# Kernel optimization log

Hardware: AMD Instinct MI355X
Metric: run time of the kernel (lower is better)

The kernel has to match this reference:

```python
import jax, jax.numpy as jnp
import numpy as np

B, T, C = 2, 2048, 2048
H, KVH, HD = 16, 4, 128  # heads, kv heads, head_dim
G = H // KVH             # GQA group size
THETA = 10000.0


def _rope_cos_sin(t, hd, dtype):
    inv_freq = 1.0 / (THETA ** (jnp.arange(0, hd, 2, dtype=jnp.float32) / hd))
    pos = jnp.arange(t, dtype=jnp.float32)
    freqs = pos[:, None] * inv_freq[None, :]          # [T, hd/2]
    emb = jnp.concatenate([freqs, freqs], axis=-1)    # [T, hd]
    return jnp.cos(emb).astype(dtype), jnp.sin(emb).astype(dtype)


def _rotate_half(x):
    x1, x2 = jnp.split(x, 2, axis=-1)
    return jnp.concatenate([-x2, x1], axis=-1)


def setup_inputs() -> dict:
    key = jax.random.key(0)
    ks = jax.random.split(key, 5)
    s_in = 1.0 / np.sqrt(C)
    return {
        "x": jax.random.normal(ks[0], (B, T, C), jnp.float32),
        "wq": jax.random.normal(ks[1], (C, H * HD), jnp.float32) * s_in,
        "bq": jnp.zeros((H * HD,), jnp.float32),
        "wk": jax.random.normal(ks[2], (C, KVH * HD), jnp.float32) * s_in,
        "bk": jnp.zeros((KVH * HD,), jnp.float32),
        "wv": jax.random.normal(ks[3], (C, KVH * HD), jnp.float32) * s_in,
        "bv": jnp.zeros((KVH * HD,), jnp.float32),
        "wo": jax.random.normal(ks[4], (H * HD, C), jnp.float32) * (1.0 / np.sqrt(H * HD)),
    }


def reference(x, wq, bq, wk, bk, wv, bv, wo):
    b, t, c = x.shape
    q = (x @ wq + bq).reshape(b, t, H, HD).transpose(0, 2, 1, 3)    # [B,H,T,hd]
    k = (x @ wk + bk).reshape(b, t, KVH, HD).transpose(0, 2, 1, 3)  # [B,KVH,T,hd]
    v = (x @ wv + bv).reshape(b, t, KVH, HD).transpose(0, 2, 1, 3)

    cos, sin = _rope_cos_sin(t, HD, x.dtype)  # [T,hd]
    q = q * cos + _rotate_half(q) * sin
    k = k * cos + _rotate_half(k) * sin

    # GQA: group query heads over kv heads
    qg = q.reshape(b, KVH, G, t, HD)
    scale = 1.0 / np.sqrt(HD)
    scores = jnp.einsum('bkgtd,bksd->bkgts', qg, k) * scale  # [B,KVH,G,T,T]
    causal = jnp.tril(jnp.ones((t, t), bool))
    scores = jnp.where(causal, scores, jnp.finfo(scores.dtype).min)
    attn = jax.nn.softmax(scores, axis=-1)
    out = jnp.einsum('bkgts,bksd->bkgtd', attn, v)            # [B,KVH,G,T,hd]
    out = out.reshape(b, H, t, HD).transpose(0, 2, 1, 3).reshape(b, t, H * HD)
    return out @ wo
```

## Files before the change

### kernel.cpp

```cpp
#include <hip/hip_runtime.h>
#include <hip/hip_bf16.h>
#include <math.h>

#define B_ 2
#define T_ 2048
#define C_ 2048
#define H_ 16
#define KVH_ 4
#define HD_ 128
#define G_ (H_ / KVH_)
#define MROWS (B_ * T_)
#define NQKV (H_ * HD_ + 2 * KVH_ * HD_)
#define KOFF (H_ * HD_)
#define VOFF (H_ * HD_ + KVH_ * HD_)

typedef __hip_bfloat16 bf16;
typedef short bf16x8 __attribute__((ext_vector_type(8)));
typedef short bf16x4 __attribute__((ext_vector_type(4)));
typedef float f32x4 __attribute__((ext_vector_type(4)));

__device__ __forceinline__ void gload_lds16(const void* g, void* l) {
  __builtin_amdgcn_global_load_lds(
      (const __attribute__((address_space(1))) unsigned int*)g,
      (__attribute__((address_space(3))) unsigned int*)l, 16, 0, 0);
}

static __device__ __forceinline__ f32x4 mfma16(bf16x4 a, bf16x4 b, f32x4 c) {
#if __has_builtin(__builtin_amdgcn_mfma_f32_16x16x16_bf16)
  return __builtin_amdgcn_mfma_f32_16x16x16_bf16(a, b, c, 0, 0, 0);
#else
  return __builtin_amdgcn_mfma_f32_16x16x16bf16_1k(a, b, c, 0, 0, 0);
#endif
}

static __device__ __forceinline__ short f2bf(float x) {
  unsigned u = __builtin_bit_cast(unsigned, x);
  u += 0x7FFFu + ((u >> 16) & 1u);
  return (short)(u >> 16);
}

static __device__ __forceinline__ float fexp2(float x) {
#if __has_builtin(__builtin_amdgcn_exp2f)
  return __builtin_amdgcn_exp2f(x);
#else
  return exp2f(x);
#endif
}

__global__ void cast_bf16_kernel(const float* __restrict__ in, bf16* __restrict__ out, int n) {
  int i = (blockIdx.x * 256 + threadIdx.x) * 4;
  if (i >= n) return;
  float4 v = *(const float4*)(in + i);
  out[i + 0] = __float2bfloat16(v.x);
  out[i + 1] = __float2bfloat16(v.y);
  out[i + 2] = __float2bfloat16(v.z);
  out[i + 3] = __float2bfloat16(v.w);
}

__global__ __launch_bounds__(256) void transpose_cast(const float* __restrict__ in,
                                                      bf16* __restrict__ out,
                                                      int R, int Ccols) {
  __shared__ float t[32][33];
  const int tx = threadIdx.x & 31, ty = threadIdx.x >> 5;
  const int r0 = blockIdx.y * 32, c0 = blockIdx.x * 32;
#pragma unroll
  for (int it = 0; it < 4; ++it)
    t[ty + 8 * it][tx] = in[(size_t)(r0 + ty + 8 * it) * Ccols + c0 + tx];
  __syncthreads();
#pragma unroll
  for (int it = 0; it < 4; ++it)
    out[(size_t)(c0 + ty + 8 * it) * R + r0 + tx] = __float2bfloat16(t[tx][ty + 8 * it]);
}

__global__ __launch_bounds__(256) void transpose_cast_qkvw(
    const float* __restrict__ wq, const float* __restrict__ wk,
    const float* __restrict__ wv, bf16* __restrict__ outT) {
  __shared__ float t[32][33];
  const int tx = threadIdx.x & 31, ty = threadIdx.x >> 5;
  const int r0 = blockIdx.y * 32;
  const int c0 = blockIdx.x * 32;
  const float* src;
  int nn, ld;
  if (c0 < KOFF)      { src = wq; nn = c0;        ld = 2048; }
  else if (c0 < VOFF) { src = wk; nn = c0 - KOFF; ld = 512; }
  else                { src = wv; nn = c0 - VOFF; ld = 512; }
#pragma unroll
  for (int it = 0; it < 4; ++it)
    t[ty + 8 * it][tx] = src[(size_t)(r0 + ty + 8 * it) * ld + nn + tx];
  __syncthreads();
#pragma unroll
  for (int it = 0; it < 4; ++it)
    outT[(size_t)(c0 + ty + 8 * it) * 2048 + r0 + tx] = __float2bfloat16(t[tx][ty + 8 * it]);
}

__global__ __launch_bounds__(256) void transpose_v(const bf16* __restrict__ qkv,
                                                   bf16* __restrict__ vt) {
  __shared__ bf16 t[32][33];
  const int tx = threadIdx.x & 31, ty = threadIdx.x >> 5;
  const int b = blockIdx.z >> 2, kvh = blockIdx.z & 3;
  const int t0 = blockIdx.x * 32, d0 = blockIdx.y * 32;
#pragma unroll
  for (int it = 0; it < 4; ++it)
    t[ty + 8 * it][tx] =
        qkv[(size_t)(b * T_ + t0 + ty + 8 * it) * NQKV + VOFF + kvh * HD_ + d0 + tx];
  __syncthreads();
#pragma unroll
  for (int it = 0; it < 4; ++it)
    vt[((size_t)((b * KVH_ + kvh) * HD_) + d0 + ty + 8 * it) * T_ + t0 + tx] =
        t[tx][ty + 8 * it];
}

__global__ void rope_bf16(bf16* __restrict__ buf, int ld, int col0, int nheads) {
  const int row = blockIdx.x / nheads;
  const int h = blockIdx.x % nheads;
  const int t = row % T_;
  const int d = threadIdx.x;
  bf16* rp = buf + (size_t)row * ld + col0 + h * HD_;
  float vd = __bfloat162float(rp[d]);
  float vp = __bfloat162float(rp[d ^ 64]);
  __syncthreads();
  const int i = d & 63;
  float invf = fexp2(-(float)i * (13.287712379549449f / 64.0f));
  float ang = (float)t * invf;
  float s, c;
  __sincosf(ang, &s, &c);
  rp[d] = __float2bfloat16((d < 64) ? (vd * c - vp * s) : (vd * c + vp * s));
}

template <bool BF16OUT>
__global__ __launch_bounds__(256, 2) void gemm_mfma(
    const bf16* __restrict__ A, const bf16* __restrict__ Bt, void* __restrict__ Cout,
    const float* __restrict__ bq, const float* __restrict__ bk2,
    const float* __restrict__ bv2, int M, int N, int K) {
  __shared__ __align__(16) bf16 As[128 * 32];
  __shared__ __align__(16) bf16 Bs[128 * 32];
  const int tid = threadIdx.x;
  const int w = tid >> 6, lane = tid & 63;
  const int colL = lane & 15, quad = lane >> 4;
  const int wm = w & 1, wn = w >> 1;
  const int r0 = blockIdx.y * 128, c0 = blockIdx.x * 128;

  f32x4 acc[4][4];
  const f32x4 zero = {0.f, 0.f, 0.f, 0.f};
#pragma unroll
  for (int mt = 0; mt < 4; ++mt)
#pragma unroll
    for (int nt = 0; nt < 4; ++nt) acc[mt][nt] = zero;

  for (int k0 = 0; k0 < K; k0 += 32) {
    __syncthreads();
#pragma unroll
    for (int it = 0; it < 2; ++it) {
      const int seg = it * 4 + w;
      const int idx = seg * 64 + lane;
      const int row = idx >> 2, off = idx & 3;
      gload_lds16(A + (size_t)(r0 + row) * K + k0 + off * 8, &As[seg * 512]);
      gload_lds16(Bt + (size_t)(c0 + row) * K + k0 + off * 8, &Bs[seg * 512]);
    }
    __syncthreads();
    bf16x8 af[4], bfv[4];
#pragma unroll
    for (int mt = 0; mt < 4; ++mt)
      af[mt] = *(const bf16x8*)&As[(wm * 64 + mt * 16 + colL) * 32 + quad * 8];
#pragma unroll
    for (int nt = 0; nt < 4; ++nt)
      bfv[nt] = *(const bf16x8*)&Bs[(wn * 64 + nt * 16 + colL) * 32 + quad * 8];
#pragma unroll
    for (int mt = 0; mt < 4; ++mt)
#pragma unroll
      for (int nt = 0; nt < 4; ++nt)
        acc[mt][nt] =
            __builtin_amdgcn_mfma_f32_16x16x32_bf16(af[mt], bfv[nt], acc[mt][nt], 0, 0, 0);
  }

#pragma unroll
  for (int nt = 0; nt < 4; ++nt) {
    const int c = c0 + wn * 64 + nt * 16 + colL;
    float bias = 0.f;
    if (bq) bias = (c < KOFF) ? bq[c] : (c < VOFF ? bk2[c - KOFF] : bv2[c - VOFF]);
#pragma unroll
    for (int mt = 0; mt < 4; ++mt) {
#pragma unroll
      for (int i = 0; i < 4; ++i) {
        const int r = r0 + wm * 64 + mt * 16 + quad * 4 + i;
        const float v = acc[mt][nt][i] + bias;
        if (BF16OUT)
          ((bf16*)Cout)[(size_t)r * N + c] = __float2bfloat16(v);
        else
          ((float*)Cout)[(size_t)r * N + c] = v;
      }
    }
  }
}

#define FA_SCL2 (0.08838834764831845f * 1.4426950408889634f)
#define FA_M2 16.0f

__global__ __launch_bounds__(128, 2) void flash_mfma5(
    const bf16* __restrict__ qkv, const bf16* __restrict__ vt, bf16* __restrict__ ao) {
  __shared__ __align__(16) char smem[32768];
  bf16* Kb0 = (bf16*)smem;
  bf16* Kb1 = (bf16*)(smem + 8192);
  bf16* Vb0 = (bf16*)(smem + 16384);
  bf16* Vb1 = (bf16*)(smem + 24576);

  const int id = blockIdx.x;
  const int hb = id >> 5;
  const int qq = id & 31;
  const int qt = (qq & 1) ? (qq >> 1) : (31 - (qq >> 1));
  const int h = hb & 15, b = hb >> 4;
  const int kvh = h >> 2;

  const int tid = threadIdx.x;
  const int w = tid >> 6, lane = tid & 63;
  const int colL = lane & 15, quad = lane >> 4;
  const int myq0 = qt * 64 + 32 * w;

  const bf16* kg = qkv + (size_t)(b * T_) * NQKV + KOFF + kvh * HD_;
  const bf16* vg = vt + (size_t)((b * KVH_ + kvh) * HD_) * T_;

  auto stageKV = [&](int tile, bf16* kl, bf16* vl) {
    const int s0k = tile * 32;
#pragma unroll
    for (int j = 0; j < 4; ++j) {
      const int s = 4 * w + j;
      const int row = s * 4 + quad;
      const int g = colL ^ (row & 7);
      gload_lds16(kg + (size_t)(s0k + row) * NQKV + g * 8, kl + s * 512);
    }
#pragma unroll
    for (int j = 0; j < 4; ++j) {
      const int s = 4 * w + j;
      const int row = s * 16 + (lane >> 2);
      const int g = (lane & 3) ^ ((row >> 1) & 3);
      gload_lds16(vg + (size_t)row * T_ + s0k + g * 8, vl + s * 512);
    }
  };

  bf16x8 qf[2][4];
  {
    const bf16* qgw = qkv + (size_t)(b * T_ + myq0) * NQKV + h * HD_;
#pragma unroll
    for (int mq = 0; mq < 2; ++mq)
#pragma unroll
      for (int c = 0; c < 4; ++c)
        qf[mq][c] = *(const bf16x8*)(qgw + (size_t)(mq * 16 + colL) * NQKV + c * 32 + quad * 8);
  }

  f32x4 o[2][8];
  const f32x4 zero = {0.f, 0.f, 0.f, 0.f};
#pragma unroll
  for (int mq = 0; mq < 2; ++mq)
#pragma unroll
    for (int ht = 0; ht < 8; ++ht) o[mq][ht] = zero;
  float l_[2] = {0.f, 0.f};

  const int nkv = 2 * qt + 2;
  stageKV(0, Kb0, Vb0);
  asm volatile("s_waitcnt vmcnt(0)\n\ts_barrier" ::: "memory");

  for (int tt = 0; tt < nkv; ++tt) {
    const bf16* Ks = (tt & 1) ? Kb1 : Kb0;
    const bf16* Vs = (tt & 1) ? Vb1 : Vb0;
    if (tt + 1 < nkv) stageKV(tt + 1, (tt & 1) ? Kb0 : Kb1, (tt & 1) ? Vb0 : Vb1);

    const int s0 = tt * 32;
    if (s0 < myq0 + 32) {
      f32x4 s_[2][2];
      s_[0][0] = zero; s_[0][1] = zero; s_[1][0] = zero; s_[1][1] = zero;
#pragma unroll
      for (int c = 0; c < 4; ++c) {
        const int ch = ((c * 4 + quad) ^ (colL & 7)) * 8;
        bf16x8 kf0 = *(const bf16x8*)(Ks + (size_t)colL * 128 + ch);
        bf16x8 kf1 = *(const bf16x8*)(Ks + (size_t)(16 + colL) * 128 + ch);
#pragma unroll
        for (int mq = 0; mq < 2; ++mq) {
          s_[0][mq] = __builtin_amdgcn_mfma_f32_16x16x32_bf16(kf0, qf[mq][c], s_[0][mq], 0, 0, 0);
          s_[1][mq] = __builtin_amdgcn_mfma_f32_16x16x32_bf16(kf1, qf[mq][c], s_[1][mq], 0, 0, 0);
        }
      }

      bf16x4 pf[2][2];
      if (s0 >= myq0) {
#pragma unroll
        for (int kt = 0; kt < 2; ++kt)
#pragma unroll
          for (int mq = 0; mq < 2; ++mq) {
            const int qcol = myq0 + mq * 16 + colL;
            const int kb = s0 + kt * 16 + quad * 4;
            float pv[4];
#pragma unroll
            for (int i = 0; i < 4; ++i) {
              float e = fexp2(fmaf(s_[kt][mq][i], FA_SCL2, -FA_M2));
              pv[i] = (kb + i <= qcol) ? e : 0.f;
            }
            l_[mq] += (pv[0] + pv[1]) + (pv[2] + pv[3]);
            pf[kt][mq] = (bf16x4){f2bf(pv[0]), f2bf(pv[1]), f2bf(pv[2]), f2bf(pv[3])};
          }
      } else {
#pragma unroll
        for (int kt = 0; kt < 2; ++kt)
#pragma unroll
          for (int mq = 0; mq < 2; ++mq) {
            float pv[4];
#pragma unroll
            for (int i = 0; i < 4; ++i)
              pv[i] = fexp2(fmaf(s_[kt][mq][i], FA_SCL2, -FA_M2));
            l_[mq] += (pv[0] + pv[1]) + (pv[2] + pv[3]);
            pf[kt][mq] = (bf16x4){f2bf(pv[0]), f2bf(pv[1]), f2bf(pv[2]), f2bf(pv[3])};
          }
      }

#pragma unroll
      for (int ht = 0; ht < 8; ++ht) {
        const int row = ht * 16 + colL;
#pragma unroll
        for (int kt = 0; kt < 2; ++kt) {
          bf16x4 vf = *(const bf16x4*)(Vs + (size_t)row * 32 +
                                       (((kt * 2 + (quad >> 1)) ^ ((row >> 1) & 3)) * 8) +
                                       (quad & 1) * 4);
#pragma unroll
          for (int mq = 0; mq < 2; ++mq) o[mq][ht] = mfma16(vf, pf[kt][mq], o[mq][ht]);
        }
      }
    }
    asm volatile("s_waitcnt vmcnt(0)\n\ts_barrier" ::: "memory");
  }

#pragma unroll
  for (int mq = 0; mq < 2; ++mq) {
    l_[mq] += __shfl_xor(l_[mq], 16);
    l_[mq] += __shfl_xor(l_[mq], 32);
    const float rl = 1.f / l_[mq];
    const size_t rbase = (size_t)(b * T_ + myq0 + mq * 16 + colL) * (H_ * HD_) + h * HD_;
#pragma unroll
    for (int ht = 0; ht < 8; ++ht) {
      bf16x4 ov;
#pragma unroll
      for (int i = 0; i < 4; ++i) ov[i] = f2bf(o[mq][ht][i] * rl);
      *(bf16x4*)(ao + rbase + ht * 16 + quad * 4) = ov;
    }
  }
}

extern "C" void kernel_launch(void* const* d_in, const int* in_sizes, int n_in,
                              void* d_out, int out_size, void* d_ws, size_t ws_size,
                              hipStream_t stream) {
  (void)in_sizes; (void)n_in; (void)out_size; (void)ws_size;
  const float* x  = (const float*)d_in[0];
  const float* wq = (const float*)d_in[1];
  const float* bq = (const float*)d_in[2];
  const float* wk = (const float*)d_in[3];
  const float* bk = (const float*)d_in[4];
  const float* wv = (const float*)d_in[5];
  const float* bv = (const float*)d_in[6];
  const float* wo = (const float*)d_in[7];
  float* out = (float*)d_out;

  char* ws = (char*)d_ws;
  bf16* xb    = (bf16*)ws;
  bf16* wqkvT = (bf16*)(ws + (16u << 20));
  bf16* woT   = (bf16*)(ws + (28u << 20));
  bf16* qkv   = (bf16*)(ws + (36u << 20));
  bf16* vt    = (bf16*)(ws + (60u << 20));

  cast_bf16_kernel<<<dim3(MROWS * C_ / 1024), dim3(256), 0, stream>>>(x, xb, MROWS * C_);

  transpose_cast_qkvw<<<dim3(96, 64), dim3(256), 0, stream>>>(wq, wk, wv, wqkvT);
  transpose_cast<<<dim3(64, 64), dim3(256), 0, stream>>>(wo, woT, 2048, 2048);

  gemm_mfma<true><<<dim3(NQKV / 128, MROWS / 128), dim3(256), 0, stream>>>(
      xb, wqkvT, qkv, bq, bk, bv, MROWS, NQKV, C_);

  rope_bf16<<<dim3(MROWS * H_), dim3(128), 0, stream>>>(qkv, NQKV, 0, H_);
  rope_bf16<<<dim3(MROWS * KVH_), dim3(128), 0, stream>>>(qkv, NQKV, KOFF, KVH_);

  transpose_v<<<dim3(T_ / 32, HD_ / 32, B_ * KVH_), dim3(256), 0, stream>>>(qkv, vt);

  bf16* ao = xb;
  flash_mfma5<<<dim3(1024), dim3(128), 0, stream>>>(qkv, vt, ao);

  gemm_mfma<false><<<dim3(C_ / 128, MROWS / 128), dim3(256), 0, stream>>>(
      ao, woT, out, nullptr, nullptr, nullptr, MROWS, C_, KOFF);
}
```

Baseline: 354.1 us.

## Pair causal query tiles per block, triple-buffer KV loads, merge RoPE launches

The flash-attention kernel now has each block handle two query tiles, qq and 31-qq, in sequence. This balances causal work per block and halves the grid to 512 blocks. KV staging moves from double to triple buffering with a partial vmcnt wait, so two tiles are in flight, and occupancy hints rise to 4 blocks/CU with 48KB LDS. The Q and K RoPE launches are merged into one launch covering 20 heads per row. The trade-offs are more LDS per block and fewer blocks, which could cut parallelism on a device with many CUs.

New measurement: 355.2 us. Within noise of the previous version (+0.3%).

```diff
diff --git a/kernel.cpp b/kernel.cpp
--- a/kernel.cpp
+++ b/kernel.cpp
@@ -110,12 +110,12 @@
         t[tx][ty + 8 * it];
 }
 
-__global__ void rope_bf16(bf16* __restrict__ buf, int ld, int col0, int nheads) {
-  const int row = blockIdx.x / nheads;
-  const int h = blockIdx.x % nheads;
+__global__ void rope_bf16(bf16* __restrict__ buf) {
+  const int row = blockIdx.x / 20;
+  const int hh = blockIdx.x % 20;
   const int t = row % T_;
   const int d = threadIdx.x;
-  bf16* rp = buf + (size_t)row * ld + col0 + h * HD_;
+  bf16* rp = buf + (size_t)row * NQKV + hh * HD_;
   float vd = __bfloat162float(rp[d]);
   float vp = __bfloat162float(rp[d ^ 64]);
   __syncthreads();
@@ -196,30 +196,26 @@
 #define FA_SCL2 (0.08838834764831845f * 1.4426950408889634f)
 #define FA_M2 16.0f
 
-__global__ __launch_bounds__(128, 2) void flash_mfma5(
+__global__ __launch_bounds__(128, 4) void flash_mfma6(
     const bf16* __restrict__ qkv, const bf16* __restrict__ vt, bf16* __restrict__ ao) {
-  __shared__ __align__(16) char smem[32768];
-  bf16* Kb0 = (bf16*)smem;
-  bf16* Kb1 = (bf16*)(smem + 8192);
-  bf16* Vb0 = (bf16*)(smem + 16384);
-  bf16* Vb1 = (bf16*)(smem + 24576);
+  __shared__ __align__(16) char smem[49152];
 
   const int id = blockIdx.x;
-  const int hb = id >> 5;
-  const int qq = id & 31;
-  const int qt = (qq & 1) ? (qq >> 1) : (31 - (qq >> 1));
+  const int hb = id >> 4;
+  const int qq = id & 15;
   const int h = hb & 15, b = hb >> 4;
   const int kvh = h >> 2;
 
   const int tid = threadIdx.x;
   const int w = tid >> 6, lane = tid & 63;
   const int colL = lane & 15, quad = lane >> 4;
-  const int myq0 = qt * 64 + 32 * w;
 
   const bf16* kg = qkv + (size_t)(b * T_) * NQKV + KOFF + kvh * HD_;
   const bf16* vg = vt + (size_t)((b * KVH_ + kvh) * HD_) * T_;
 
-  auto stageKV = [&](int tile, bf16* kl, bf16* vl) {
+  auto stageKV = [&](int tile, char* base) {
+    bf16* kl = (bf16*)base;
+    bf16* vl = (bf16*)(base + 8192);
     const int s0k = tile * 32;
 #pragma unroll
     for (int j = 0; j < 4; ++j) {
@@ -237,108 +233,125 @@
     }
   };
 
-  bf16x8 qf[2][4];
-  {
-    const bf16* qgw = qkv + (size_t)(b * T_ + myq0) * NQKV + h * HD_;
+#pragma unroll 1
+  for (int pass = 0; pass < 2; ++pass) {
+    const int qt = pass ? (31 - qq) : qq;
+    const int myq0 = qt * 64 + 32 * w;
+    const int nkv = 2 * qt + 2;
+
+    bf16x8 qf[2][4];
+    {
+      const bf16* qgw = qkv + (size_t)(b * T_ + myq0) * NQKV + h * HD_;
+#pragma unroll
+      for (int mq = 0; mq < 2; ++mq)
+#pragma unroll
+        for (int c = 0; c < 4; ++c)
+          qf[mq][c] = *(const bf16x8*)(qgw + (size_t)(mq * 16 + colL) * NQKV + c * 32 + quad * 8);
+    }
+
+    f32x4 o[2][8];
+    const f32x4 zero = {0.f, 0.f, 0.f, 0.f};
 #pragma unroll
     for (int mq = 0; mq < 2; ++mq)
 #pragma unroll
-      for (int c = 0; c < 4; ++c)
-        qf[mq][c] = *(const bf16x8*)(qgw + (size_t)(mq * 16 + colL) * NQKV + c * 32 + quad * 8);
-  }
-
-  f32x4 o[2][8];
-  const f32x4 zero = {0.f, 0.f, 0.f, 0.f};
-#pragma unroll
-  for (int mq = 0; mq < 2; ++mq)
-#pragma unroll
-    for (int ht = 0; ht < 8; ++ht) o[mq][ht] = zero;
-  float l_[2] = {0.f, 0.f};
-
-  const int nkv = 2 * qt + 2;
-  stageKV(0, Kb0, Vb0);
-  asm volatile("s_waitcnt vmcnt(0)\n\ts_barrier" ::: "memory");
-
-  for (int tt = 0; tt < nkv; ++tt) {
-    const bf16* Ks = (tt & 1) ? Kb1 : Kb0;
-    const bf16* Vs = (tt & 1) ? Vb1 : Vb0;
-    if (tt + 1 < nkv) stageKV(tt + 1, (tt & 1) ? Kb0 : Kb1, (tt & 1) ? Vb0 : Vb1);
-
-    const int s0 = tt * 32;
-    if (s0 < myq0 + 32) {
-      f32x4 s_[2][2];
-      s_[0][0] = zero; s_[0][1] = zero; s_[1][0] = zero; s_[1][1] = zero;
-#pragma unroll
-      for (int c = 0; c < 4; ++c) {
-        const int ch = ((c * 4 + quad) ^ (colL & 7)) * 8;
-        bf16x8 kf0 = *(const bf16x8*)(Ks + (size_t)colL * 128 + ch);
-        bf16x8 kf1 = *(const bf16x8*)(Ks + (size_t)(16 + colL) * 128 + ch);
-#pragma unroll
-        for (int mq = 0; mq < 2; ++mq) {
-          s_[0][mq] = __builtin_amdgcn_mfma_f32_16x16x32_bf16(kf0, qf[mq][c], s_[0][mq], 0, 0, 0);
-          s_[1][mq] = __builtin_amdgcn_mfma_f32_16x16x32_bf16(kf1, qf[mq][c], s_[1][mq], 0, 0, 0);
+      for (int ht = 0; ht < 8; ++ht) o[mq][ht] = zero;
+    float l_[2] = {0.f, 0.f};
+
+    stageKV(0, smem);
+    stageKV(1, smem + 16384);
+    asm volatile("s_waitcnt vmcnt(8)\n\ts_barrier" ::: "memory");
+
+    int rb = 0, sb = 2;
+#pragma unroll 1
+    for (int tt = 0; tt < nkv; ++tt) {
+      const bool pre = (tt + 2 < nkv);
+      if (pre) stageKV(tt + 2, smem + sb * 16384);
+      const bf16* Ks = (const bf16*)(smem + rb * 16384);
+      const bf16* Vs = (const bf16*)(smem + rb * 16384 + 8192);
+
+      const int s0 = tt * 32;
+      if (s0 < myq0 + 32) {
+        f32x4 s_[2][2];
+        s_[0][0] = zero; s_[0][1] = zero; s_[1][0] = zero; s_[1][1] = zero;
+#pragma unroll
+        for (int c = 0; c < 4; ++c) {
+          const int ch = ((c * 4 + quad) ^ (colL & 7)) * 8;
+          bf16x8 kf0 = *(const bf16x8*)(Ks + (size_t)colL * 128 + ch);
+          bf16x8 kf1 = *(const bf16x8*)(Ks + (size_t)(16 + colL) * 128 + ch);
+#pragma unroll
+          for (int mq = 0; mq < 2; ++mq) {
+            s_[0][mq] = __builtin_amdgcn_mfma_f32_16x16x32_bf16(kf0, qf[mq][c], s_[0][mq], 0, 0, 0);
+            s_[1][mq] = __builtin_amdgcn_mfma_f32_16x16x32_bf16(kf1, qf[mq][c], s_[1][mq], 0, 0, 0);
+          }
+        }
+
+        bf16x4 pf[2][2];
+        if (s0 >= myq0) {
+#pragma unroll
+          for (int kt = 0; kt < 2; ++kt)
+#pragma unroll
+            for (int mq = 0; mq < 2; ++mq) {
+              const int qcol = myq0 + mq * 16 + colL;
+              const int kb = s0 + kt * 16 + quad * 4;
+              float pv[4];
+#pragma unroll
+              for (int i = 0; i < 4; ++i) {
+                float e = fexp2(fmaf(s_[kt][mq][i], FA_SCL2, -FA_M2));
+                pv[i] = (kb + i <= qcol) ? e : 0.f;
+              }
+              l_[mq] += (pv[0] + pv[1]) + (pv[2] + pv[3]);
+              pf[kt][mq] = (bf16x4){f2bf(pv[0]), f2bf(pv[1]), f2bf(pv[2]), f2bf(pv[3])};
+            }
+        } else {
+#pragma unroll
+          for (int kt = 0; kt < 2; ++kt)
+#pragma unroll
+            for (int mq = 0; mq < 2; ++mq) {
+              float pv[4];
+#pragma unroll
+              for (int i = 0; i < 4; ++i)
+                pv[i] = fexp2(fmaf(s_[kt][mq][i], FA_SCL2, -FA_M2));
+              l_[mq] += (pv[0] + pv[1]) + (pv[2] + pv[3]);
+              pf[kt][mq] = (bf16x4){f2bf(pv[0]), f2bf(pv[1]), f2bf(pv[2]), f2bf(pv[3])};
+            }
+        }
+
+#pragma unroll
+        for (int ht = 0; ht < 8; ++ht) {
+          const int row = ht * 16 + colL;
+#pragma unroll
+          for (int kt = 0; kt < 2; ++kt) {
+            bf16x4 vf = *(const bf16x4*)(Vs + (size_t)row * 32 +
+                                         (((kt * 2 + (quad >> 1)) ^ ((row >> 1) & 3)) * 8) +
+                                         (quad & 1) * 4);
+#pragma unroll
+            for (int mq = 0; mq < 2; ++mq) o[mq][ht] = mfma16(vf, pf[kt][mq], o[mq][ht]);
+          }
         }
       }
 
-      bf16x4 pf[2][2];
-      if (s0 >= myq0) {
-#pragma unroll
-        for (int kt = 0; kt < 2; ++kt)
-#pragma unroll
-          for (int mq = 0; mq < 2; ++mq) {
-            const int qcol = myq0 + mq * 16 + colL;
-            const int kb = s0 + kt * 16 + quad * 4;
-            float pv[4];
-#pragma unroll
-            for (int i = 0; i < 4; ++i) {
-              float e = fexp2(fmaf(s_[kt][mq][i], FA_SCL2, -FA_M2));
-              pv[i] = (kb + i <= qcol) ? e : 0.f;
-            }
-            l_[mq] += (pv[0] + pv[1]) + (pv[2] + pv[3]);
-            pf[kt][mq] = (bf16x4){f2bf(pv[0]), f2bf(pv[1]), f2bf(pv[2]), f2bf(pv[3])};
-          }
-      } else {
-#pragma unroll
-        for (int kt = 0; kt < 2; ++kt)
-#pragma unroll
-          for (int mq = 0; mq < 2; ++mq) {
-            float pv[4];
-#pragma unroll
-            for (int i = 0; i < 4; ++i)
-              pv[i] = fexp2(fmaf(s_[kt][mq][i], FA_SCL2, -FA_M2));
-            l_[mq] += (pv[0] + pv[1]) + (pv[2] + pv[3]);
-            pf[kt][mq] = (bf16x4){f2bf(pv[0]), f2bf(pv[1]), f2bf(pv[2]), f2bf(pv[3])};
-          }
+      if (pre)
+        asm volatile("s_waitcnt vmcnt(8)\n\ts_barrier" ::: "memory");
+      else
+        asm volatile("s_waitcnt vmcnt(0)\n\ts_barrier" ::: "memory");
+      rb = (rb == 2) ? 0 : rb + 1;
+      sb = (sb == 2) ? 0 : sb + 1;
+    }
+
+#pragma unroll
+    for (int mq = 0; mq < 2; ++mq) {
+      float lv = l_[mq];
+      lv += __shfl_xor(lv, 16);
+      lv += __shfl_xor(lv, 32);
+      const float rl = 1.f / lv;
+      const size_t rbase = (size_t)(b * T_ + myq0 + mq * 16 + colL) * (H_ * HD_) + h * HD_;
+#pragma unroll
+      for (int ht = 0; ht < 8; ++ht) {
+        bf16x4 ov;
+#pragma unroll
+        for (int i = 0; i < 4; ++i) ov[i] = f2bf(o[mq][ht][i] * rl);
+        *(bf16x4*)(ao + rbase + ht * 16 + quad * 4) = ov;
       }
-
-#pragma unroll
-      for (int ht = 0; ht < 8; ++ht) {
-        const int row = ht * 16 + colL;
-#pragma unroll
-        for (int kt = 0; kt < 2; ++kt) {
-          bf16x4 vf = *(const bf16x4*)(Vs + (size_t)row * 32 +
-                                       (((kt * 2 + (quad >> 1)) ^ ((row >> 1) & 3)) * 8) +
-                                       (quad & 1) * 4);
-#pragma unroll
-          for (int mq = 0; mq < 2; ++mq) o[mq][ht] = mfma16(vf, pf[kt][mq], o[mq][ht]);
-        }
-      }
-    }
-    asm volatile("s_waitcnt vmcnt(0)\n\ts_barrier" ::: "memory");
-  }
-
-#pragma unroll
-  for (int mq = 0; mq < 2; ++mq) {
-    l_[mq] += __shfl_xor(l_[mq], 16);
-    l_[mq] += __shfl_xor(l_[mq], 32);
-    const float rl = 1.f / l_[mq];
-    const size_t rbase = (size_t)(b * T_ + myq0 + mq * 16 + colL) * (H_ * HD_) + h * HD_;
-#pragma unroll
-    for (int ht = 0; ht < 8; ++ht) {
-      bf16x4 ov;
-#pragma unroll
-      for (int i = 0; i < 4; ++i) ov[i] = f2bf(o[mq][ht][i] * rl);
-      *(bf16x4*)(ao + rbase + ht * 16 + quad * 4) = ov;
     }
   }
 }
@@ -372,13 +385,12 @@
   gemm_mfma<true><<<dim3(NQKV / 128, MROWS / 128), dim3(256), 0, stream>>>(
       xb, wqkvT, qkv, bq, bk, bv, MROWS, NQKV, C_);
 
-  rope_bf16<<<dim3(MROWS * H_), dim3(128), 0, stream>>>(qkv, NQKV, 0, H_);
-  rope_bf16<<<dim3(MROWS * KVH_), dim3(128), 0, stream>>>(qkv, NQKV, KOFF, KVH_);
+  rope_bf16<<<dim3(MROWS * 20), dim3(128), 0, stream>>>(qkv);
 
   transpose_v<<<dim3(T_ / 32, HD_ / 32, B_ * KVH_), dim3(256), 0, stream>>>(qkv, vt);
 
   bf16* ao = xb;
-  flash_mfma5<<<dim3(1024), dim3(128), 0, stream>>>(qkv, vt, ao);
+  flash_mfma6<<<dim3(512), dim3(128), 0, stream>>>(qkv, vt, ao);
 
   gemm_mfma<false><<<dim3(C_ / 128, MROWS / 128), dim3(256), 0, stream>>>(
       ao, woT, out, nullptr, nullptr, nullptr, MROWS, C_, KOFF);
```
